# Performance work log

Hardware: AMD Instinct MI355X
Metric: run time of the kernel (lower is better)

## Reference

```python
import jax, jax.numpy as jnp
import numpy as np

B, M, D, H = 32, 1024, 768, 256


def setup_inputs() -> dict:
    key = jax.random.key(0)
    k = jax.random.split(key, 6)
    V = jax.random.normal(k[0], (B, M, D), dtype=jnp.float32)
    alpha = jnp.float32(0.5)
    # torch nn.Linear weights: [out, in]
    WV_w = jax.random.normal(k[1], (H, D), dtype=jnp.float32) * (1.0 / np.sqrt(D))
    WV_b = jnp.zeros((H,), dtype=jnp.float32)
    W_conv = jax.random.normal(k[2], (H, H), dtype=jnp.float32) * (1.0 / np.sqrt(H))
    res_w = jax.random.normal(k[3], (H, D), dtype=jnp.float32) * (1.0 / np.sqrt(D))
    res_b = jnp.zeros((H,), dtype=jnp.float32)
    return {"V": V, "alpha": alpha, "WV_w": WV_w, "WV_b": WV_b,
            "W_conv": W_conv, "res_w": res_w, "res_b": res_b}


def reference(V, alpha, WV_w, WV_b, W_conv, res_w, res_b):
    # global feature awareness enhancement: alpha*V + (1-alpha)*mean
    g = jnp.mean(V, axis=1, keepdims=True)            # [B,1,D]
    V_enh = alpha * V + (1.0 - alpha) * g             # [B,M,D]
    # projection (torch Linear: x @ W.T + b)
    Vp = jnp.einsum('bmd,hd->bmh', V_enh, WV_w) + WV_b  # [B,M,H]
    # dynamic incidence matrix: row-softmax of Vp @ Vp.T
    sim = jnp.einsum('bmh,bnh->bmn', Vp, Vp)          # [B,M,M]
    H_TV = jax.nn.softmax(sim, axis=-1)               # [B,M,M]
    # hypergraph convolution: H @ ((H.T @ X) @ W)
    t1 = jnp.einsum('bnm,bnh->bmh', H_TV, Vp)         # H.T @ X -> [B,M,H]
    t2 = jnp.einsum('bmh,hk->bmk', t1, W_conv)        # [B,M,H]
    O = jnp.einsum('bmn,bnh->bmh', H_TV, t2)          # [B,M,H]
    # residual projection + relu
    res = jnp.einsum('bmd,hd->bmh', V, res_w) + res_b  # [B,M,H]
    return jax.nn.relu(O + res)
```

## Files before the change

kernel.cpp:

```cpp
#include <hip/hip_runtime.h>
#include <math.h>


typedef __attribute__((ext_vector_type(8))) short bf16x8;
typedef __attribute__((ext_vector_type(4))) float f32x4;

__device__ __forceinline__ ushort f2b(float f) {
    unsigned u = __float_as_uint(f);
    return (ushort)((u + 0x7fffu + ((u >> 16) & 1u)) >> 16);
}
__device__ __forceinline__ float b2f(ushort u) {
    return __uint_as_float((unsigned)u << 16);
}
__device__ __forceinline__ uint4 pack8(float4 a, float4 b) {
    uint4 r;
    r.x = f2b(a.x) | ((unsigned)f2b(a.y) << 16);
    r.y = f2b(a.z) | ((unsigned)f2b(a.w) << 16);
    r.z = f2b(b.x) | ((unsigned)f2b(b.y) << 16);
    r.w = f2b(b.z) | ((unsigned)f2b(b.w) << 16);
    return r;
}

__device__ __forceinline__ void gl16(const void* g, void* l) {
    __builtin_amdgcn_global_load_lds(
        (__attribute__((address_space(1))) const unsigned*)g,
        (__attribute__((address_space(3))) unsigned*)l, 16, 0, 0);
}

__device__ __forceinline__ void gemm_core(const ushort* __restrict__ A,
                                          const ushort* __restrict__ Bt,
                                          int K, ushort* As, ushort* Bs,
                                          f32x4 acc[4][4]) {
    const int tid = threadIdx.x;
    const int lane = tid & 63;
    const int wave = tid >> 6;
    const int l8 = lane >> 3, l7 = lane & 7;
    const int swz = ((l7 ^ l8) << 4);
    const char* pa[4];
    const char* pb[4];
    ushort* la[4];
    ushort* lb[4];
    #pragma unroll
    for (int i = 0; i < 4; ++i) {
        int r = (wave * 4 + i) * 8 + l8;
        pa[i] = (const char*)A + (size_t)r * (K * 2) + swz;
        pb[i] = (const char*)Bt + (size_t)r * (K * 2) + swz;
        la[i] = As + (wave * 4 + i) * 512;
        lb[i] = Bs + (wave * 4 + i) * 512;
    }
    const int rr = lane & 15;
    const int kq = (lane >> 4) << 4;
    const int mask = (rr & 7) << 4;
    const int c0 = kq ^ mask;
    const int c1 = (64 + kq) ^ mask;
    const int wr = (wave >> 1) * 64, wc = (wave & 1) * 64;
    const int arow0 = (wr + rr) * 128, brow0 = (wc + rr) * 128;

    for (int k0 = 0; k0 < K; k0 += 64) {
        __syncthreads();
        #pragma unroll
        for (int i = 0; i < 4; ++i) {
            gl16(pa[i], la[i]);
            gl16(pb[i], lb[i]);
            pa[i] += 128; pb[i] += 128;
        }
        __syncthreads();
        #pragma unroll
        for (int ks = 0; ks < 2; ++ks) {
            const int cc = ks ? c1 : c0;
            bf16x8 av[4], bv[4];
            #pragma unroll
            for (int i = 0; i < 4; ++i) {
                av[i] = *(const bf16x8*)((const char*)As + arow0 + i * 2048 + cc);
                bv[i] = *(const bf16x8*)((const char*)Bs + brow0 + i * 2048 + cc);
            }
            #pragma unroll
            for (int i = 0; i < 4; ++i)
                #pragma unroll
                for (int j = 0; j < 4; ++j)
                    acc[i][j] = __builtin_amdgcn_mfma_f32_16x16x32_bf16(av[i], bv[j], acc[i][j], 0, 0, 0);
        }
    }
}

#define EPI_COORDS \
    const int lane = threadIdx.x & 63; \
    const int wave = threadIdx.x >> 6; \
    const int rb = (wave >> 1) * 64 + (lane >> 4) * 4; \
    const int cb = (wave & 1) * 64 + (lane & 15);

__global__ __launch_bounds__(192) void k_castmean(const float* __restrict__ V,
                                                  ushort* __restrict__ Vb,
                                                  float* __restrict__ gpart) {
    const int b = blockIdx.x, mc = blockIdx.y, t = threadIdx.x;
    const size_t base = ((size_t)(b * 1024 + mc * 128)) * 768 + t * 4;
    const float* src = V + base;
    ushort* dst = Vb + base;
    float4 s = make_float4(0.f, 0.f, 0.f, 0.f);
    for (int r = 0; r < 128; ++r) {
        float4 v = *(const float4*)(src + (size_t)r * 768);
        s.x += v.x; s.y += v.y; s.z += v.z; s.w += v.w;
        unsigned u0 = f2b(v.x) | ((unsigned)f2b(v.y) << 16);
        unsigned u1 = f2b(v.z) | ((unsigned)f2b(v.w) << 16);
        *(uint2*)(dst + (size_t)r * 768) = make_uint2(u0, u1);
    }
    *(float4*)&gpart[(size_t)(mc * 32 + b) * 768 + t * 4] = s;
}

__global__ __launch_bounds__(256) void k_gsum(const float* __restrict__ gpart, float* __restrict__ g) {
    int idx = blockIdx.x * 256 + threadIdx.x;
    float s = 0.f;
    #pragma unroll
    for (int c = 0; c < 8; ++c) s += gpart[(size_t)c * 24576 + idx];
    g[idx] = s * (1.0f / 1024.0f);
}

__global__ __launch_bounds__(256) void k_gW(const float* __restrict__ g,
                                            const float* __restrict__ WVw,
                                            float* __restrict__ gW) {
    int idx = blockIdx.x * 256 + threadIdx.x;
    int b = idx >> 8, h = idx & 255;
    const float* gr = g + b * 768;
    const float* wr = WVw + (size_t)h * 768;
    float s = 0.f;
    for (int d = 0; d < 768; ++d) s += gr[d] * wr[d];
    gW[idx] = s;
}

__global__ __launch_bounds__(256) void k_castw(const float* __restrict__ WVw,
                                               const float* __restrict__ resw,
                                               ushort* __restrict__ Wcat) {
    int id = blockIdx.x * 256 + threadIdx.x;
    int n = id / 96, c = (id - n * 96) * 8;
    const float* src = (n < 256) ? (WVw + (size_t)n * 768 + c) : (resw + (size_t)(n - 256) * 768 + c);
    *(uint4*)(Wcat + (size_t)n * 768 + c) = pack8(*(const float4*)src, *(const float4*)(src + 4));
}

__global__ __launch_bounds__(256) void k_wct(const float* __restrict__ Wc, ushort* __restrict__ WcT) {
    __shared__ float t[64][65];
    const int r0 = blockIdx.y * 64, c0 = blockIdx.x * 64;
    const int tid = threadIdx.x;
    #pragma unroll
    for (int i = 0; i < 4; ++i) {
        int r = (tid >> 4) + i * 16, c4 = (tid & 15) * 4;
        float4 v = *(const float4*)&Wc[(size_t)(r0 + r) * 256 + c0 + c4];
        t[r][c4] = v.x; t[r][c4 + 1] = v.y; t[r][c4 + 2] = v.z; t[r][c4 + 3] = v.w;
    }
    __syncthreads();
    #pragma unroll
    for (int i = 0; i < 4; ++i) {
        int oc = (tid >> 4) + i * 16, r4 = (tid & 15) * 4;
        unsigned lo = f2b(t[r4][oc]) | ((unsigned)f2b(t[r4 + 1][oc]) << 16);
        unsigned hi = f2b(t[r4 + 2][oc]) | ((unsigned)f2b(t[r4 + 3][oc]) << 16);
        *(uint2*)&WcT[(size_t)(c0 + oc) * 256 + r0 + r4] = make_uint2(lo, hi);
    }
}

__global__ __launch_bounds__(256) void k_proj(const ushort* __restrict__ Vb, const ushort* __restrict__ Wcat,
                                              const float* __restrict__ WVb, const float* __restrict__ resb,
                                              const float* __restrict__ gW, const float* __restrict__ alpha_p,
                                              ushort* __restrict__ Vp, ushort* __restrict__ resv) {
    __shared__ ushort As[128 * 64], Bs[128 * 64];
    f32x4 acc[4][4] = {};
    const int n0 = blockIdx.x * 128, m0 = blockIdx.y * 128;
    gemm_core(Vb + (size_t)m0 * 768, Wcat + (size_t)n0 * 768, 768, As, Bs, acc);
    EPI_COORDS
    const float alpha = *alpha_p, oma = 1.0f - alpha;
    #pragma unroll
    for (int i = 0; i < 4; ++i)
        #pragma unroll
        for (int j = 0; j < 4; ++j) {
            int gcol = n0 + cb + j * 16;
            #pragma unroll
            for (int r = 0; r < 4; ++r) {
                int grow = m0 + rb + i * 16 + r;
                float v = acc[i][j][r];
                if (gcol < 256) {
                    float o = alpha * v + oma * gW[((grow >> 10) << 8) + gcol] + WVb[gcol];
                    Vp[(size_t)grow * 256 + gcol] = f2b(o);
                } else {
                    resv[(size_t)grow * 256 + gcol - 256] = f2b(v + resb[gcol - 256]);
                }
            }
        }
}

__global__ __launch_bounds__(256) void k_rownorm(const ushort* __restrict__ Vp, float* __restrict__ rn) {
    const int row = blockIdx.x * 4 + (threadIdx.x >> 6);
    const int lane = threadIdx.x & 63;
    uint2 v = *(const uint2*)(Vp + (size_t)row * 256 + lane * 4);
    float f0 = b2f((ushort)(v.x & 0xffff)), f1 = b2f((ushort)(v.x >> 16));
    float f2 = b2f((ushort)(v.y & 0xffff)), f3 = b2f((ushort)(v.y >> 16));
    float s = f0 * f0 + f1 * f1 + f2 * f2 + f3 * f3;
    #pragma unroll
    for (int o = 32; o > 0; o >>= 1) s += __shfl_xor(s, o, 64);
    if (lane == 0) rn[row] = s;
}

__global__ __launch_bounds__(256) void k_shift(const float* __restrict__ rn, float* __restrict__ shift) {
    const int b = blockIdx.x, tid = threadIdx.x;
    const float* p = rn + b * 1024;
    float m = fmaxf(fmaxf(p[tid], p[tid + 256]), fmaxf(p[tid + 512], p[tid + 768]));
    #pragma unroll
    for (int o = 32; o > 0; o >>= 1) m = fmaxf(m, __shfl_xor(m, o, 64));
    __shared__ float red[4];
    if ((tid & 63) == 0) red[tid >> 6] = m;
    __syncthreads();
    if (tid == 0)
        shift[b] = fmaxf(fmaxf(red[0], red[1]), fmaxf(red[2], red[3]));
}

__global__ __launch_bounds__(256) void k_sim(const ushort* __restrict__ Vp,
                                             const float* __restrict__ shift,
                                             ushort* __restrict__ E,
                                             float* __restrict__ Z) {
    __shared__ ushort As[128 * 64], Bs[128 * 64];
    f32x4 acc[4][4] = {};
    const int b = blockIdx.z;
    const ushort* Vb_ = Vp + (size_t)b * 1024 * 256;
    const int n0 = blockIdx.x * 128, m0 = blockIdx.y * 128;
    gemm_core(Vb_ + (size_t)m0 * 256, Vb_ + (size_t)n0 * 256, 256, As, Bs, acc);
    ushort* Eb = E + ((size_t)b << 20);
    const float sh = shift[b];
    EPI_COORDS
    #pragma unroll
    for (int i = 0; i < 4; ++i)
        #pragma unroll
        for (int r = 0; r < 4; ++r) {
            const int row = m0 + rb + i * 16 + r;
            float e[4];
            float s = 0.f;
            #pragma unroll
            for (int j = 0; j < 4; ++j) {
                e[j] = __expf(acc[i][j][r] - sh);
                s += e[j];
                Eb[(size_t)row * 1024 + n0 + cb + j * 16] = f2b(e[j]);
            }
            s += __shfl_xor(s, 1, 64);
            s += __shfl_xor(s, 2, 64);
            s += __shfl_xor(s, 4, 64);
            s += __shfl_xor(s, 8, 64);
            if ((lane & 15) == 0)
                atomicAdd(&Z[b * 1024 + row], s);
        }
}

__global__ __launch_bounds__(256) void k_trbs(const ushort* __restrict__ Vp,
                                              const float* __restrict__ Z,
                                              ushort* __restrict__ VpZT) {
    __shared__ ushort t[64][68];
    const int b = blockIdx.z;
    const ushort* ib = Vp + (size_t)b * 1024 * 256;
    ushort* ob = VpZT + (size_t)b * 256 * 1024;
    const int c0 = blockIdx.x * 64, r0 = blockIdx.y * 64;
    const int tid = threadIdx.x;
    #pragma unroll
    for (int i = 0; i < 4; ++i) {
        int r = (tid >> 4) + i * 16, c4 = (tid & 15) * 4;
        uint2 v = *(const uint2*)(ib + (size_t)(r0 + r) * 256 + c0 + c4);
        float iz = 1.0f / Z[b * 1024 + r0 + r];
        unsigned lo = f2b(b2f((ushort)(v.x & 0xffff)) * iz) |
                      ((unsigned)f2b(b2f((ushort)(v.x >> 16)) * iz) << 16);
        unsigned hi = f2b(b2f((ushort)(v.y & 0xffff)) * iz) |
                      ((unsigned)f2b(b2f((ushort)(v.y >> 16)) * iz) << 16);
        *(uint2*)&t[r][c4] = make_uint2(lo, hi);
    }
    __syncthreads();
    #pragma unroll
    for (int i = 0; i < 4; ++i) {
        int oc = (tid >> 4) + i * 16, r4 = (tid & 15) * 4;
        unsigned lo = t[r4][oc] | ((unsigned)t[r4 + 1][oc] << 16);
        unsigned hi = t[r4 + 2][oc] | ((unsigned)t[r4 + 3][oc] << 16);
        *(uint2*)(ob + (size_t)(c0 + oc) * 1024 + r0 + r4) = make_uint2(lo, hi);
    }
}

__global__ __launch_bounds__(256) void k_trb(const ushort* __restrict__ in, ushort* __restrict__ out) {
    __shared__ ushort t[64][68];
    const int b = blockIdx.z;
    const ushort* ib = in + (size_t)b * 1024 * 256;
    ushort* ob = out + (size_t)b * 256 * 1024;
    const int c0 = blockIdx.x * 64, r0 = blockIdx.y * 64;
    const int tid = threadIdx.x;
    #pragma unroll
    for (int i = 0; i < 4; ++i) {
        int r = (tid >> 4) + i * 16, c4 = (tid & 15) * 4;
        *(uint2*)&t[r][c4] = *(const uint2*)(ib + (size_t)(r0 + r) * 256 + c0 + c4);
    }
    __syncthreads();
    #pragma unroll
    for (int i = 0; i < 4; ++i) {
        int oc = (tid >> 4) + i * 16, r4 = (tid & 15) * 4;
        unsigned lo = t[r4][oc] | ((unsigned)t[r4 + 1][oc] << 16);
        unsigned hi = t[r4 + 2][oc] | ((unsigned)t[r4 + 3][oc] << 16);
        *(uint2*)(ob + (size_t)(c0 + oc) * 1024 + r0 + r4) = make_uint2(lo, hi);
    }
}

__global__ __launch_bounds__(256) void k_t1(const ushort* __restrict__ E, const ushort* __restrict__ VpZT,
                                            ushort* __restrict__ t1) {
    __shared__ ushort As[128 * 64], Bs[128 * 64];
    f32x4 acc[4][4] = {};
    const int b = blockIdx.z;
    const int n0 = blockIdx.x * 128, m0 = blockIdx.y * 128;
    gemm_core(E + ((size_t)b << 20) + (size_t)m0 * 1024,
              VpZT + (size_t)b * 256 * 1024 + (size_t)n0 * 1024, 1024, As, Bs, acc);
    ushort* ob = t1 + (size_t)b * 1024 * 256;
    EPI_COORDS
    #pragma unroll
    for (int i = 0; i < 4; ++i)
        #pragma unroll
        for (int j = 0; j < 4; ++j)
            #pragma unroll
            for (int r = 0; r < 4; ++r)
                ob[(size_t)(m0 + rb + i * 16 + r) * 256 + n0 + cb + j * 16] = f2b(acc[i][j][r]);
}

__global__ __launch_bounds__(256) void k_t2(const ushort* __restrict__ t1, const ushort* __restrict__ WcT,
                                            ushort* __restrict__ t2) {
    __shared__ ushort As[128 * 64], Bs[128 * 64];
    f32x4 acc[4][4] = {};
    const int n0 = blockIdx.x * 128, m0 = blockIdx.y * 128;
    gemm_core(t1 + (size_t)m0 * 256, WcT + (size_t)n0 * 256, 256, As, Bs, acc);
    EPI_COORDS
    #pragma unroll
    for (int i = 0; i < 4; ++i)
        #pragma unroll
        for (int j = 0; j < 4; ++j)
            #pragma unroll
            for (int r = 0; r < 4; ++r)
                t2[(size_t)(m0 + rb + i * 16 + r) * 256 + n0 + cb + j * 16] = f2b(acc[i][j][r]);
}

__global__ __launch_bounds__(256) void k_O(const ushort* __restrict__ E, const ushort* __restrict__ t2T,
                                           const ushort* __restrict__ resv, const float* __restrict__ Z,
                                           float* __restrict__ out) {
    __shared__ ushort As[128 * 64], Bs[128 * 64];
    f32x4 acc[4][4] = {};
    const int b = blockIdx.z;
    const int n0 = blockIdx.x * 128, m0 = blockIdx.y * 128;
    gemm_core(E + ((size_t)b << 20) + (size_t)m0 * 1024,
              t2T + (size_t)b * 256 * 1024 + (size_t)n0 * 1024, 1024, As, Bs, acc);
    EPI_COORDS
    #pragma unroll
    for (int i = 0; i < 4; ++i)
        #pragma unroll
        for (int j = 0; j < 4; ++j)
            #pragma unroll
            for (int r = 0; r < 4; ++r) {
                int row = m0 + rb + i * 16 + r;
                float iz = 1.0f / Z[b * 1024 + row];
                size_t off = ((size_t)(b * 1024 + row)) * 256 + n0 + cb + j * 16;
                out[off] = fmaxf(acc[i][j][r] * iz + b2f(resv[off]), 0.0f);
            }
}

extern "C" void kernel_launch(void* const* d_in, const int* in_sizes, int n_in,
                              void* d_out, int out_size, void* d_ws, size_t ws_size,
                              hipStream_t stream) {
    const float* V     = (const float*)d_in[0];
    const float* alpha = (const float*)d_in[1];
    const float* WVw   = (const float*)d_in[2];
    const float* WVb   = (const float*)d_in[3];
    const float* Wc    = (const float*)d_in[4];
    const float* resw  = (const float*)d_in[5];
    const float* resb  = (const float*)d_in[6];
    float* out = (float*)d_out;

    char* W = (char*)d_ws;
    ushort* Vb   = (ushort*)(W);
    ushort* E    = (ushort*)(W + (48ull  << 20));
    ushort* Vp   = (ushort*)(W + (112ull << 20));
    ushort* resv = (ushort*)(W + (128ull << 20));
    ushort* VpZT = (ushort*)(W + (144ull << 20));
    ushort* t1   = (ushort*)(W + (160ull << 20));
    ushort* t2   = (ushort*)(W + (176ull << 20));
    ushort* t2T  = (ushort*)(W + (192ull << 20));
    ushort* Wcat = (ushort*)(W + (208ull << 20));
    ushort* WcT  = (ushort*)(W + (209ull << 20));
    float*  gpart= (float*) (W + (210ull << 20));
    float*  g    = (float*) (W + (211ull << 20));
    float*  gW   = (float*) (W + (211ull << 20) + (128u << 10));
    float*  shv  = (float*) (W + (211ull << 20) + (256u << 10));
    float*  rn   = (float*) (W + (211ull << 20) + (512u << 10));
    float*  Z    = (float*) (W + (212ull << 20));

    hipMemsetAsync(Z, 0, 32768 * sizeof(float), stream);

    k_castmean<<<dim3(32, 8), 192, 0, stream>>>(V, Vb, gpart);
    k_gsum<<<96, 256, 0, stream>>>(gpart, g);
    k_gW<<<32, 256, 0, stream>>>(g, WVw, gW);
    k_castw<<<192, 256, 0, stream>>>(WVw, resw, Wcat);
    k_wct<<<dim3(4, 4), 256, 0, stream>>>(Wc, WcT);
    k_proj<<<dim3(4, 256), 256, 0, stream>>>(Vb, Wcat, WVb, resb, gW, alpha, Vp, resv);
    k_rownorm<<<8192, 256, 0, stream>>>(Vp, rn);
    k_shift<<<32, 256, 0, stream>>>(rn, shv);
    k_sim<<<dim3(8, 8, 32), 256, 0, stream>>>(Vp, shv, E, Z);
    k_trbs<<<dim3(4, 16, 32), 256, 0, stream>>>(Vp, Z, VpZT);
    k_t1<<<dim3(2, 8, 32), 256, 0, stream>>>(E, VpZT, t1);
    k_t2<<<dim3(2, 256), 256, 0, stream>>>(t1, WcT, t2);
    k_trb<<<dim3(4, 16, 32), 256, 0, stream>>>(t2, t2T);
    k_O<<<dim3(2, 8, 32), 256, 0, stream>>>(E, t2T, resv, Z, out);
}
```

Before: 416.8 us.

## Fuse t1, t2 and transpose into one kernel and remap block order

```diff
diff --git a/kernel.cpp b/kernel.cpp
--- a/kernel.cpp
+++ b/kernel.cpp
@@ -93,11 +93,11 @@
                                                   ushort* __restrict__ Vb,
                                                   float* __restrict__ gpart) {
     const int b = blockIdx.x, mc = blockIdx.y, t = threadIdx.x;
-    const size_t base = ((size_t)(b * 1024 + mc * 128)) * 768 + t * 4;
+    const size_t base = ((size_t)(b * 1024 + mc * 64)) * 768 + t * 4;
     const float* src = V + base;
     ushort* dst = Vb + base;
     float4 s = make_float4(0.f, 0.f, 0.f, 0.f);
-    for (int r = 0; r < 128; ++r) {
+    for (int r = 0; r < 64; ++r) {
         float4 v = *(const float4*)(src + (size_t)r * 768);
         s.x += v.x; s.y += v.y; s.z += v.z; s.w += v.w;
         unsigned u0 = f2b(v.x) | ((unsigned)f2b(v.y) << 16);
@@ -111,7 +111,7 @@
     int idx = blockIdx.x * 256 + threadIdx.x;
     float s = 0.f;
     #pragma unroll
-    for (int c = 0; c < 8; ++c) s += gpart[(size_t)c * 24576 + idx];
+    for (int c = 0; c < 16; ++c) s += gpart[(size_t)c * 24576 + idx];
     g[idx] = s * (1.0f / 1024.0f);
 }
 
@@ -162,19 +162,20 @@
                                               ushort* __restrict__ Vp, ushort* __restrict__ resv) {
     __shared__ ushort As[128 * 64], Bs[128 * 64];
     f32x4 acc[4][4] = {};
-    const int n0 = blockIdx.x * 128, m0 = blockIdx.y * 128;
+    const int j = (blockIdx.x & 7) * 128 + (blockIdx.x >> 3);
+    const int n0 = (j & 3) * 128, m0 = (j >> 2) * 128;
     gemm_core(Vb + (size_t)m0 * 768, Wcat + (size_t)n0 * 768, 768, As, Bs, acc);
     EPI_COORDS
     const float alpha = *alpha_p, oma = 1.0f - alpha;
     #pragma unroll
     for (int i = 0; i < 4; ++i)
         #pragma unroll
-        for (int j = 0; j < 4; ++j) {
-            int gcol = n0 + cb + j * 16;
+        for (int jj = 0; jj < 4; ++jj) {
+            int gcol = n0 + cb + jj * 16;
             #pragma unroll
             for (int r = 0; r < 4; ++r) {
                 int grow = m0 + rb + i * 16 + r;
-                float v = acc[i][j][r];
+                float v = acc[i][jj][r];
                 if (gcol < 256) {
                     float o = alpha * v + oma * gW[((grow >> 10) << 8) + gcol] + WVb[gcol];
                     Vp[(size_t)grow * 256 + gcol] = f2b(o);
@@ -216,9 +217,9 @@
                                              float* __restrict__ Z) {
     __shared__ ushort As[128 * 64], Bs[128 * 64];
     f32x4 acc[4][4] = {};
-    const int b = blockIdx.z;
+    const int j = (blockIdx.x & 7) * 256 + (blockIdx.x >> 3);
+    const int n0 = (j & 7) * 128, m0 = ((j >> 3) & 7) * 128, b = j >> 6;
     const ushort* Vb_ = Vp + (size_t)b * 1024 * 256;
-    const int n0 = blockIdx.x * 128, m0 = blockIdx.y * 128;
     gemm_core(Vb_ + (size_t)m0 * 256, Vb_ + (size_t)n0 * 256, 256, As, Bs, acc);
     ushort* Eb = E + ((size_t)b << 20);
     const float sh = shift[b];
@@ -231,10 +232,10 @@
             float e[4];
             float s = 0.f;
             #pragma unroll
-            for (int j = 0; j < 4; ++j) {
-                e[j] = __expf(acc[i][j][r] - sh);
-                s += e[j];
-                Eb[(size_t)row * 1024 + n0 + cb + j * 16] = f2b(e[j]);
+            for (int jj = 0; jj < 4; ++jj) {
+                e[jj] = __expf(acc[i][jj][r] - sh);
+                s += e[jj];
+                Eb[(size_t)row * 1024 + n0 + cb + jj * 16] = f2b(e[jj]);
             }
             s += __shfl_xor(s, 1, 64);
             s += __shfl_xor(s, 2, 64);
@@ -275,61 +276,121 @@
     }
 }
 
-__global__ __launch_bounds__(256) void k_trb(const ushort* __restrict__ in, ushort* __restrict__ out) {
-    __shared__ ushort t[64][68];
-    const int b = blockIdx.z;
-    const ushort* ib = in + (size_t)b * 1024 * 256;
-    ushort* ob = out + (size_t)b * 256 * 1024;
-    const int c0 = blockIdx.x * 64, r0 = blockIdx.y * 64;
+__global__ __launch_bounds__(512) void k_t12(const ushort* __restrict__ E,
+                                             const ushort* __restrict__ VpZT,
+                                             const ushort* __restrict__ WcT,
+                                             ushort* __restrict__ t2T) {
+    __shared__ char smem[65536];
+    char* Asb = smem;
+    char* Bsb = smem + 16384;
+
+    const int j = (blockIdx.x & 7) * 32 + (blockIdx.x >> 3);
+    const int m0 = (j & 7) * 128;
+    const int b = j >> 3;
+    const ushort* Eb = E + ((size_t)b << 20) + (size_t)m0 * 1024;
+    const ushort* Vz = VpZT + (size_t)b * 256 * 1024;
     const int tid = threadIdx.x;
-    #pragma unroll
-    for (int i = 0; i < 4; ++i) {
-        int r = (tid >> 4) + i * 16, c4 = (tid & 15) * 4;
-        *(uint2*)&t[r][c4] = *(const uint2*)(ib + (size_t)(r0 + r) * 256 + c0 + c4);
-    }
-    __syncthreads();
-    #pragma unroll
-    for (int i = 0; i < 4; ++i) {
-        int oc = (tid >> 4) + i * 16, r4 = (tid & 15) * 4;
-        unsigned lo = t[r4][oc] | ((unsigned)t[r4 + 1][oc] << 16);
-        unsigned hi = t[r4 + 2][oc] | ((unsigned)t[r4 + 3][oc] << 16);
-        *(uint2*)(ob + (size_t)(c0 + oc) * 1024 + r0 + r4) = make_uint2(lo, hi);
-    }
-}
-
-__global__ __launch_bounds__(256) void k_t1(const ushort* __restrict__ E, const ushort* __restrict__ VpZT,
-                                            ushort* __restrict__ t1) {
-    __shared__ ushort As[128 * 64], Bs[128 * 64];
+    const int lane = tid & 63, wave = tid >> 6;
+    const int l8 = lane >> 3, l7 = lane & 7;
+    const int swz = (l7 ^ l8) << 4;
+
+    const char* pa[2]; char* la[2];
+    const char* pb[4]; char* lb[4];
+    #pragma unroll
+    for (int ii = 0; ii < 2; ++ii) {
+        int r = wave * 16 + ii * 8 + l8;
+        pa[ii] = (const char*)(Eb + (size_t)r * 1024) + swz;
+        la[ii] = Asb + (wave * 16 + ii * 8) * 128;
+    }
+    #pragma unroll
+    for (int ii = 0; ii < 4; ++ii) {
+        int r = wave * 32 + ii * 8 + l8;
+        pb[ii] = (const char*)(Vz + (size_t)r * 1024) + swz;
+        lb[ii] = Bsb + (wave * 32 + ii * 8) * 128;
+    }
+    const int rr = lane & 15;
+    const int kq = (lane >> 4) << 4;
+    const int mask = (rr & 7) << 4;
+    const int wr = (wave >> 2) * 64, wc = (wave & 3) * 64;
     f32x4 acc[4][4] = {};
-    const int b = blockIdx.z;
-    const int n0 = blockIdx.x * 128, m0 = blockIdx.y * 128;
-    gemm_core(E + ((size_t)b << 20) + (size_t)m0 * 1024,
-              VpZT + (size_t)b * 256 * 1024 + (size_t)n0 * 1024, 1024, As, Bs, acc);
-    ushort* ob = t1 + (size_t)b * 1024 * 256;
-    EPI_COORDS
+    for (int k0 = 0; k0 < 1024; k0 += 64) {
+        __syncthreads();
+        #pragma unroll
+        for (int ii = 0; ii < 2; ++ii) { gl16(pa[ii], la[ii]); pa[ii] += 128; }
+        #pragma unroll
+        for (int ii = 0; ii < 4; ++ii) { gl16(pb[ii], lb[ii]); pb[ii] += 128; }
+        __syncthreads();
+        #pragma unroll
+        for (int ks = 0; ks < 2; ++ks) {
+            const int cc = (ks * 64 + kq) ^ mask;
+            bf16x8 av[4], bv[4];
+            #pragma unroll
+            for (int i = 0; i < 4; ++i) {
+                av[i] = *(const bf16x8*)(Asb + (wr + i * 16 + rr) * 128 + cc);
+                bv[i] = *(const bf16x8*)(Bsb + (wc + i * 16 + rr) * 128 + cc);
+            }
+            #pragma unroll
+            for (int i = 0; i < 4; ++i)
+                #pragma unroll
+                for (int jj = 0; jj < 4; ++jj)
+                    acc[i][jj] = __builtin_amdgcn_mfma_f32_16x16x32_bf16(av[i], bv[jj], acc[i][jj], 0, 0, 0);
+        }
+    }
+    __syncthreads();
+    const int rb = wr + (lane >> 4) * 4;
+    const int cbh = wc + (lane & 15);
     #pragma unroll
     for (int i = 0; i < 4; ++i)
         #pragma unroll
-        for (int j = 0; j < 4; ++j)
-            #pragma unroll
-            for (int r = 0; r < 4; ++r)
-                ob[(size_t)(m0 + rb + i * 16 + r) * 256 + n0 + cb + j * 16] = f2b(acc[i][j][r]);
-}
-
-__global__ __launch_bounds__(256) void k_t2(const ushort* __restrict__ t1, const ushort* __restrict__ WcT,
-                                            ushort* __restrict__ t2) {
-    __shared__ ushort As[128 * 64], Bs[128 * 64];
-    f32x4 acc[4][4] = {};
-    const int n0 = blockIdx.x * 128, m0 = blockIdx.y * 128;
-    gemm_core(t1 + (size_t)m0 * 256, WcT + (size_t)n0 * 256, 256, As, Bs, acc);
-    EPI_COORDS
+        for (int jj = 0; jj < 4; ++jj) {
+            int h = cbh + jj * 16;
+            #pragma unroll
+            for (int r = 0; r < 4; ++r) {
+                int m = rb + i * 16 + r;
+                *(ushort*)(smem + m * 512 + ((2 * h) ^ ((m & 7) << 4))) = f2b(acc[i][jj][r]);
+            }
+        }
+    __syncthreads();
+    f32x4 acc2[4][4] = {};
+    #pragma unroll
+    for (int k2 = 0; k2 < 4; ++k2) {
+        #pragma unroll
+        for (int ks = 0; ks < 2; ++ks) {
+            const int cbyte = k2 * 128 + ks * 64 + kq;
+            bf16x8 av[4], bv[4];
+            #pragma unroll
+            for (int i = 0; i < 4; ++i) {
+                int m = wr + i * 16 + rr;
+                av[i] = *(const bf16x8*)(smem + m * 512 + (cbyte ^ ((m & 7) << 4)));
+                int h = wc + i * 16 + rr;
+                bv[i] = *(const bf16x8*)((const char*)WcT + h * 512 + cbyte);
+            }
+            #pragma unroll
+            for (int i = 0; i < 4; ++i)
+                #pragma unroll
+                for (int jj = 0; jj < 4; ++jj)
+                    acc2[i][jj] = __builtin_amdgcn_mfma_f32_16x16x32_bf16(av[i], bv[jj], acc2[i][jj], 0, 0, 0);
+        }
+    }
+    __syncthreads();
     #pragma unroll
     for (int i = 0; i < 4; ++i)
         #pragma unroll
-        for (int j = 0; j < 4; ++j)
-            #pragma unroll
-            for (int r = 0; r < 4; ++r)
-                t2[(size_t)(m0 + rb + i * 16 + r) * 256 + n0 + cb + j * 16] = f2b(acc[i][j][r]);
+        for (int jj = 0; jj < 4; ++jj) {
+            int h = cbh + jj * 16;
+            int m = rb + i * 16;
+            unsigned u0 = f2b(acc2[i][jj][0]) | ((unsigned)f2b(acc2[i][jj][1]) << 16);
+            unsigned u1 = f2b(acc2[i][jj][2]) | ((unsigned)f2b(acc2[i][jj][3]) << 16);
+            *(uint2*)(smem + h * 256 + ((2 * m) ^ ((h & 7) << 4))) = make_uint2(u0, u1);
+        }
+    __syncthreads();
+    ushort* ob = t2T + (size_t)b * 256 * 1024 + m0;
+    const int h = tid >> 1, mh = (tid & 1) * 64;
+    #pragma unroll
+    for (int i = 0; i < 8; ++i) {
+        uint4 v = *(const uint4*)(smem + h * 256 + (((mh + i * 8) * 2) ^ ((h & 7) << 4)));
+        *(uint4*)(ob + (size_t)h * 1024 + mh + i * 8) = v;
+    }
 }
 
 __global__ __launch_bounds__(256) void k_O(const ushort* __restrict__ E, const ushort* __restrict__ t2T,
@@ -337,21 +398,21 @@
                                            float* __restrict__ out) {
     __shared__ ushort As[128 * 64], Bs[128 * 64];
     f32x4 acc[4][4] = {};
-    const int b = blockIdx.z;
-    const int n0 = blockIdx.x * 128, m0 = blockIdx.y * 128;
+    const int j = (blockIdx.x & 7) * 64 + (blockIdx.x >> 3);
+    const int n0 = (j & 1) * 128, m0 = ((j >> 1) & 7) * 128, b = j >> 4;
     gemm_core(E + ((size_t)b << 20) + (size_t)m0 * 1024,
               t2T + (size_t)b * 256 * 1024 + (size_t)n0 * 1024, 1024, As, Bs, acc);
     EPI_COORDS
     #pragma unroll
     for (int i = 0; i < 4; ++i)
         #pragma unroll
-        for (int j = 0; j < 4; ++j)
+        for (int jj = 0; jj < 4; ++jj)
             #pragma unroll
             for (int r = 0; r < 4; ++r) {
                 int row = m0 + rb + i * 16 + r;
                 float iz = 1.0f / Z[b * 1024 + row];
-                size_t off = ((size_t)(b * 1024 + row)) * 256 + n0 + cb + j * 16;
-                out[off] = fmaxf(acc[i][j][r] * iz + b2f(resv[off]), 0.0f);
+                size_t off = ((size_t)(b * 1024 + row)) * 256 + n0 + cb + jj * 16;
+                out[off] = fmaxf(acc[i][jj][r] * iz + b2f(resv[off]), 0.0f);
             }
 }
 
@@ -373,32 +434,28 @@
     ushort* Vp   = (ushort*)(W + (112ull << 20));
     ushort* resv = (ushort*)(W + (128ull << 20));
     ushort* VpZT = (ushort*)(W + (144ull << 20));
-    ushort* t1   = (ushort*)(W + (160ull << 20));
-    ushort* t2   = (ushort*)(W + (176ull << 20));
     ushort* t2T  = (ushort*)(W + (192ull << 20));
     ushort* Wcat = (ushort*)(W + (208ull << 20));
     ushort* WcT  = (ushort*)(W + (209ull << 20));
     float*  gpart= (float*) (W + (210ull << 20));
-    float*  g    = (float*) (W + (211ull << 20));
-    float*  gW   = (float*) (W + (211ull << 20) + (128u << 10));
-    float*  shv  = (float*) (W + (211ull << 20) + (256u << 10));
-    float*  rn   = (float*) (W + (211ull << 20) + (512u << 10));
-    float*  Z    = (float*) (W + (212ull << 20));
+    float*  g    = (float*) (W + (212ull << 20));
+    float*  gW   = (float*) (W + (212ull << 20) + (128u << 10));
+    float*  shv  = (float*) (W + (212ull << 20) + (256u << 10));
+    float*  rn   = (float*) (W + (212ull << 20) + (512u << 10));
+    float*  Z    = (float*) (W + (213ull << 20));
 
     hipMemsetAsync(Z, 0, 32768 * sizeof(float), stream);
 
-    k_castmean<<<dim3(32, 8), 192, 0, stream>>>(V, Vb, gpart);
+    k_castmean<<<dim3(32, 16), 192, 0, stream>>>(V, Vb, gpart);
     k_gsum<<<96, 256, 0, stream>>>(gpart, g);
     k_gW<<<32, 256, 0, stream>>>(g, WVw, gW);
     k_castw<<<192, 256, 0, stream>>>(WVw, resw, Wcat);
     k_wct<<<dim3(4, 4), 256, 0, stream>>>(Wc, WcT);
-    k_proj<<<dim3(4, 256), 256, 0, stream>>>(Vb, Wcat, WVb, resb, gW, alpha, Vp, resv);
+    k_proj<<<1024, 256, 0, stream>>>(Vb, Wcat, WVb, resb, gW, alpha, Vp, resv);
     k_rownorm<<<8192, 256, 0, stream>>>(Vp, rn);
     k_shift<<<32, 256, 0, stream>>>(rn, shv);
-    k_sim<<<dim3(8, 8, 32), 256, 0, stream>>>(Vp, shv, E, Z);
+    k_sim<<<2048, 256, 0, stream>>>(Vp, shv, E, Z);
     k_trbs<<<dim3(4, 16, 32), 256, 0, stream>>>(Vp, Z, VpZT);
-    k_t1<<<dim3(2, 8, 32), 256, 0, stream>>>(E, VpZT, t1);
-    k_t2<<<dim3(2, 256), 256, 0, stream>>>(t1, WcT, t2);
-    k_trb<<<dim3(4, 16, 32), 256, 0, stream>>>(t2, t2T);
-    k_O<<<dim3(2, 8, 32), 256, 0, stream>>>(E, t2T, resv, Z, out);
-}
+    k_t12<<<256, 512, 0, stream>>>(E, VpZT, WcT, t2T);
+    k_O<<<512, 256, 0, stream>>>(E, t2T, resv, Z, out);
+}
```

Result: faster. 384.8 us (-7.7%).
